# Optimization experiments

Measured on AMD Instinct MI355X. Metric: run time of the kernel, lower is better.

Reference implementation:

```python
import jax, jax.numpy as jnp
import numpy as np


def setup_inputs() -> dict:
    key = jax.random.key(0)
    k1, k2, k3 = jax.random.split(key, 3)
    B, S, D = 2, 2048, 4096
    x = jax.random.normal(k1, (B, S, D), dtype=jnp.float32)
    weight = jax.random.normal(k2, (D, D), dtype=jnp.float32)  # [out, in]
    bias = jax.random.normal(k3, (D,), dtype=jnp.float32)
    return {"x": x, "weight": weight, "bias": bias}


def reference(x, weight, bias):
    # STE binarization: forward uses sign(W) (sign(0)=0, matching torch.sign)
    w = jnp.sign(weight)
    # F.linear: x @ w.T + b
    return jnp.einsum('bsk,nk->bsn', x, w) + bias
```

## Files before the change

### kernel.cpp

```cpp
#include <hip/hip_runtime.h>
#include <hip/hip_bf16.h>
#include <stdint.h>

#define M_DIM 4096
#define N_DIM 4096
#define K_DIM 4096
#define BM 128
#define BN 128
#define BK 64

typedef float f32x4 __attribute__((ext_vector_type(4)));
typedef __bf16 bf16x8 __attribute__((ext_vector_type(8)));
typedef float f4 __attribute__((ext_vector_type(4)));
typedef unsigned int u32x4 __attribute__((ext_vector_type(4)));
typedef unsigned short u16x4 __attribute__((ext_vector_type(4)));

__device__ __forceinline__ uint16_t f32_to_bf16_rn(float f) {
  uint32_t u = __float_as_uint(f);
  u += 0x7fffu + ((u >> 16) & 1u);
  return (uint16_t)(u >> 16);
}

__global__ void convert_w_kernel(const u32x4* __restrict__ w4,
                                 u16x4* __restrict__ s4, int n4) {
  int idx = blockIdx.x * blockDim.x + threadIdx.x;
  int stride = gridDim.x * blockDim.x;
  for (int i = idx; i < n4; i += stride) {
    u32x4 v = w4[i];
    u16x4 o;
#pragma unroll
    for (int j = 0; j < 4; ++j) {
      uint32_t b = v[j];
      o[j] = ((b & 0x7fffffffu) == 0u)
                 ? (uint16_t)0
                 : (uint16_t)(0x3F80u | ((b >> 16) & 0x8000u));
    }
    s4[i] = o;
  }
}

__global__ void convert_x_kernel(const f4* __restrict__ x4,
                                 u16x4* __restrict__ hi4,
                                 u16x4* __restrict__ lo4, int n4) {
  int idx = blockIdx.x * blockDim.x + threadIdx.x;
  int stride = gridDim.x * blockDim.x;
  for (int i = idx; i < n4; i += stride) {
    f4 v = x4[i];
    u16x4 h, l;
#pragma unroll
    for (int j = 0; j < 4; ++j) {
      uint16_t hb = f32_to_bf16_rn(v[j]);
      float r = v[j] - __uint_as_float((uint32_t)hb << 16);
      h[j] = hb;
      l[j] = f32_to_bf16_rn(r);
    }
    hi4[i] = h;
    lo4[i] = l;
  }
}

__device__ __forceinline__ void gload_lds16(const void* g, void* l) {
  __builtin_amdgcn_global_load_lds(
      (__attribute__((address_space(1))) void*)(g),
      (__attribute__((address_space(3))) void*)(l),
      16, 0, 0);
}

__launch_bounds__(256, 3)
__global__ void bingemm_kernel(const uint16_t* __restrict__ Ahi,
                               const uint16_t* __restrict__ Alo,
                               const uint16_t* __restrict__ Bs,
                               const float* __restrict__ bias,
                               float* __restrict__ out) {
  __shared__ uint16_t sAh[BM * BK];
  __shared__ uint16_t sAl[BM * BK];
  __shared__ uint16_t sB[BN * BK];

  const int t = threadIdx.x;
  const int lane = t & 63;
  const int wave = t >> 6;
  const int wr = (wave >> 1) * 64;
  const int wc = (wave & 1) * 64;
  const int bm = blockIdx.y * BM;
  const int bn = blockIdx.x * BN;

  const int srow = t >> 3;
  const int scol = (t & 7) * 8;
  const uint16_t* gAh = Ahi + (size_t)(bm + srow) * K_DIM + scol;
  const uint16_t* gAl = Alo + (size_t)(bm + srow) * K_DIM + scol;
  const uint16_t* gB = Bs + (size_t)(bn + srow) * K_DIM + scol;

  f32x4 acc[4][4];
#pragma unroll
  for (int i = 0; i < 4; ++i)
#pragma unroll
    for (int j = 0; j < 4; ++j) acc[i][j] = (f32x4){0.f, 0.f, 0.f, 0.f};

  const int r15 = lane & 15;
  const int kgrp = (lane >> 4) * 8;

  for (int kt = 0; kt < K_DIM; kt += BK) {
#pragma unroll
    for (int i = 0; i < 4; ++i) {
      gload_lds16(gAh + kt + i * 32 * K_DIM, &sAh[t * 8 + i * 2048]);
      gload_lds16(gAl + kt + i * 32 * K_DIM, &sAl[t * 8 + i * 2048]);
      gload_lds16(gB + kt + i * 32 * K_DIM, &sB[t * 8 + i * 2048]);
    }
    __syncthreads();

#pragma unroll
    for (int ks = 0; ks < 2; ++ks) {
      const int ko = ks * 32 + kgrp;
      bf16x8 ah[4], al[4], bb[4];
#pragma unroll
      for (int i = 0; i < 4; ++i) {
        ah[i] = *(const bf16x8*)&sAh[(wr + i * 16 + r15) * BK + ko];
        al[i] = *(const bf16x8*)&sAl[(wr + i * 16 + r15) * BK + ko];
        bb[i] = *(const bf16x8*)&sB[(wc + i * 16 + r15) * BK + ko];
      }
#pragma unroll
      for (int mi = 0; mi < 4; ++mi)
#pragma unroll
        for (int ni = 0; ni < 4; ++ni) {
          acc[mi][ni] = __builtin_amdgcn_mfma_f32_16x16x32_bf16(
              ah[mi], bb[ni], acc[mi][ni], 0, 0, 0);
          acc[mi][ni] = __builtin_amdgcn_mfma_f32_16x16x32_bf16(
              al[mi], bb[ni], acc[mi][ni], 0, 0, 0);
        }
    }
    __syncthreads();
  }

  const int rowg = (lane >> 4) * 4;
#pragma unroll
  for (int ni = 0; ni < 4; ++ni) {
    const int col = bn + wc + ni * 16 + r15;
    const float bv = bias[col];
#pragma unroll
    for (int mi = 0; mi < 4; ++mi) {
      const int row0 = bm + wr + mi * 16 + rowg;
#pragma unroll
      for (int i = 0; i < 4; ++i)
        out[(size_t)(row0 + i) * N_DIM + col] = acc[mi][ni][i] + bv;
    }
  }
}

__global__ void fallback_gemm(const float* __restrict__ x,
                              const float* __restrict__ w,
                              const float* __restrict__ bias,
                              float* __restrict__ out) {
  __shared__ float sx[16][17];
  __shared__ float sw[16][17];
  int tx = threadIdx.x & 15, ty = threadIdx.x >> 4;
  int m = blockIdx.y * 16 + ty;
  int n = blockIdx.x * 16 + tx;
  float acc = 0.f;
  for (int k0 = 0; k0 < K_DIM; k0 += 16) {
    sx[ty][tx] = x[(size_t)m * K_DIM + k0 + tx];
    float wv = w[(size_t)(blockIdx.x * 16 + ty) * K_DIM + k0 + tx];
    sw[ty][tx] = (wv > 0.f) ? 1.f : ((wv < 0.f) ? -1.f : 0.f);
    __syncthreads();
#pragma unroll
    for (int kk = 0; kk < 16; ++kk) acc += sx[ty][kk] * sw[tx][kk];
    __syncthreads();
  }
  out[(size_t)m * N_DIM + n] = acc + bias[n];
}

extern "C" void kernel_launch(void* const* d_in, const int* in_sizes, int n_in,
                              void* d_out, int out_size, void* d_ws,
                              size_t ws_size, hipStream_t stream) {
  const float* x = (const float*)d_in[0];
  const float* w = (const float*)d_in[1];
  const float* bias = (const float*)d_in[2];
  float* out = (float*)d_out;

  const size_t elems = (size_t)N_DIM * K_DIM;
  const size_t need = elems * 2u * 3u;

  if (ws_size < need) {
    dim3 grid(N_DIM / 16, M_DIM / 16);
    fallback_gemm<<<grid, 256, 0, stream>>>(x, w, bias, out);
    return;
  }

  uint16_t* Sb = (uint16_t*)d_ws;
  uint16_t* Ahi = Sb + elems;
  uint16_t* Alo = Ahi + elems;

  const int n4 = (int)(elems / 4);
  convert_w_kernel<<<2048, 256, 0, stream>>>((const u32x4*)w, (u16x4*)Sb, n4);
  convert_x_kernel<<<2048, 256, 0, stream>>>((const f4*)x, (u16x4*)Ahi,
                                             (u16x4*)Alo, n4);

  dim3 grid(N_DIM / BN, M_DIM / BM);
  bingemm_kernel<<<grid, 256, 0, stream>>>(Ahi, Alo, Sb, bias, out);
}
```

Measured before the change: 428.0 us.

## Rewrite binary GEMM as 256x256 8-wave double-buffered kernel with concatenated hi/lo A

After: 402.8 us. 1.06x faster.

```diff
diff --git a/kernel.cpp b/kernel.cpp
--- a/kernel.cpp
+++ b/kernel.cpp
@@ -5,9 +5,7 @@
 #define M_DIM 4096
 #define N_DIM 4096
 #define K_DIM 4096
-#define BM 128
-#define BN 128
-#define BK 64
+#define NT 128
 
 typedef float f32x4 __attribute__((ext_vector_type(4)));
 typedef __bf16 bf16x8 __attribute__((ext_vector_type(8)));
@@ -40,8 +38,7 @@
 }
 
 __global__ void convert_x_kernel(const f4* __restrict__ x4,
-                                 u16x4* __restrict__ hi4,
-                                 u16x4* __restrict__ lo4, int n4) {
+                                 uint16_t* __restrict__ Ab, int n4) {
   int idx = blockIdx.x * blockDim.x + threadIdx.x;
   int stride = gridDim.x * blockDim.x;
   for (int i = idx; i < n4; i += stride) {
@@ -54,8 +51,11 @@
       h[j] = hb;
       l[j] = f32_to_bf16_rn(r);
     }
-    hi4[i] = h;
-    lo4[i] = l;
+    int flat = i * 4;
+    int m = flat >> 12;
+    int k = flat & 4095;
+    *(u16x4*)&Ab[(size_t)m * 8192 + k] = h;
+    *(u16x4*)&Ab[(size_t)m * 8192 + 4096 + k] = l;
   }
 }
 
@@ -66,82 +66,162 @@
       16, 0, 0);
 }
 
-__launch_bounds__(256, 3)
-__global__ void bingemm_kernel(const uint16_t* __restrict__ Ahi,
-                               const uint16_t* __restrict__ Alo,
-                               const uint16_t* __restrict__ Bs,
-                               const float* __restrict__ bias,
-                               float* __restrict__ out) {
-  __shared__ uint16_t sAh[BM * BK];
-  __shared__ uint16_t sAl[BM * BK];
-  __shared__ uint16_t sB[BN * BK];
+__global__ __launch_bounds__(512, 2)
+void bingemm8(const uint16_t* __restrict__ Ab, const uint16_t* __restrict__ Bs,
+              const float* __restrict__ bias, float* __restrict__ out) {
+  __shared__ uint16_t sA[2][2][8192];
+  __shared__ uint16_t sB[2][2][8192];
 
   const int t = threadIdx.x;
   const int lane = t & 63;
-  const int wave = t >> 6;
-  const int wr = (wave >> 1) * 64;
-  const int wc = (wave & 1) * 64;
-  const int bm = blockIdx.y * BM;
-  const int bn = blockIdx.x * BN;
+  const int w = t >> 6;
+  const int r15 = lane & 15;
+
+  const int bid = blockIdx.x;
+  const int swz = (bid & 7) * 32 + (bid >> 3);
+  const int bm = (swz >> 4) * 256;
+  const int bn = (swz & 15) * 256;
 
   const int srow = t >> 3;
-  const int scol = (t & 7) * 8;
-  const uint16_t* gAh = Ahi + (size_t)(bm + srow) * K_DIM + scol;
-  const uint16_t* gAl = Alo + (size_t)(bm + srow) * K_DIM + scol;
-  const uint16_t* gB = Bs + (size_t)(bn + srow) * K_DIM + scol;
-
-  f32x4 acc[4][4];
-#pragma unroll
-  for (int i = 0; i < 4; ++i)
-#pragma unroll
-    for (int j = 0; j < 4; ++j) acc[i][j] = (f32x4){0.f, 0.f, 0.f, 0.f};
-
-  const int r15 = lane & 15;
-  const int kgrp = (lane >> 4) * 8;
-
-  for (int kt = 0; kt < K_DIM; kt += BK) {
-#pragma unroll
-    for (int i = 0; i < 4; ++i) {
-      gload_lds16(gAh + kt + i * 32 * K_DIM, &sAh[t * 8 + i * 2048]);
-      gload_lds16(gAl + kt + i * 32 * K_DIM, &sAl[t * 8 + i * 2048]);
-      gload_lds16(gB + kt + i * 32 * K_DIM, &sB[t * 8 + i * 2048]);
-    }
-    __syncthreads();
-
-#pragma unroll
-    for (int ks = 0; ks < 2; ++ks) {
-      const int ko = ks * 32 + kgrp;
-      bf16x8 ah[4], al[4], bb[4];
-#pragma unroll
-      for (int i = 0; i < 4; ++i) {
-        ah[i] = *(const bf16x8*)&sAh[(wr + i * 16 + r15) * BK + ko];
-        al[i] = *(const bf16x8*)&sAl[(wr + i * 16 + r15) * BK + ko];
-        bb[i] = *(const bf16x8*)&sB[(wc + i * 16 + r15) * BK + ko];
-      }
-#pragma unroll
-      for (int mi = 0; mi < 4; ++mi)
-#pragma unroll
-        for (int ni = 0; ni < 4; ++ni) {
-          acc[mi][ni] = __builtin_amdgcn_mfma_f32_16x16x32_bf16(
-              ah[mi], bb[ni], acc[mi][ni], 0, 0, 0);
-          acc[mi][ni] = __builtin_amdgcn_mfma_f32_16x16x32_bf16(
-              al[mi], bb[ni], acc[mi][ni], 0, 0, 0);
-        }
-    }
-    __syncthreads();
-  }
+  const int scol = (((t & 7) ^ (srow & 7)) * 8);
+  const size_t aThr = (size_t)(bm + srow) * 8192 + scol;
+  const size_t bThr = (size_t)(bn + srow) * 4096 + scol;
+
+#define STAGE_A(KT, HH, BUF)                                        \
+  do {                                                              \
+    const uint16_t* g = Ab + aThr + (size_t)(HH) * 128 * 8192 +     \
+                        (size_t)(KT) * 64;                          \
+    gload_lds16(g, &sA[BUF][HH][t * 8]);                            \
+    gload_lds16(g + (size_t)64 * 8192, &sA[BUF][HH][t * 8 + 4096]); \
+  } while (0)
+#define STAGE_B(KT, HH, BUF)                                        \
+  do {                                                              \
+    const uint16_t* g = Bs + bThr + (size_t)(HH) * 128 * 4096 +     \
+                        (size_t)((KT) & 63) * 64;                   \
+    gload_lds16(g, &sB[BUF][HH][t * 8]);                            \
+    gload_lds16(g + (size_t)64 * 4096, &sB[BUF][HH][t * 8 + 4096]); \
+  } while (0)
+
+  const int klane = lane >> 4;
+  const int cb0 = (klane * 16) ^ ((lane & 7) << 4);
+  const int whA = w >> 2;
+  const int whB = (w & 3) >> 1;
+  const int wcl = (w & 1) * 64;
+  const int eA0 = r15 * 64 + (cb0 >> 1);
+  const int eA1 = eA0 ^ 32;
+  const int eB0 = (wcl + r15) * 64 + (cb0 >> 1);
+  const int eB1 = eB0 ^ 32;
+
+  bf16x8 rA[4][2], rB[4][2];
+  f32x4 acc[8][4];
+#pragma unroll
+  for (int m = 0; m < 8; ++m)
+#pragma unroll
+    for (int n = 0; n < 4; ++n) acc[m][n] = (f32x4){0.f, 0.f, 0.f, 0.f};
+
+#define LOAD_A(BUF, MOFF)                                            \
+  {                                                                  \
+    _Pragma("unroll") for (int m = 0; m < 4; ++m) {                  \
+      rA[m][0] = *(const bf16x8*)&sA[BUF][whA][eA0 + ((MOFF) + m) * 1024]; \
+      rA[m][1] = *(const bf16x8*)&sA[BUF][whA][eA1 + ((MOFF) + m) * 1024]; \
+    }                                                                \
+  }
+#define LOAD_B(BUF, NB)                                              \
+  {                                                                  \
+    _Pragma("unroll") for (int n = 0; n < 2; ++n) {                  \
+      rB[(NB) + n][0] = *(const bf16x8*)&sB[BUF][whB][eB0 + ((NB) + n) * 1024]; \
+      rB[(NB) + n][1] = *(const bf16x8*)&sB[BUF][whB][eB1 + ((NB) + n) * 1024]; \
+    }                                                                \
+  }
+#define MFMA_Q(MB, NB)                                               \
+  {                                                                  \
+    _Pragma("unroll") for (int mm = 0; mm < 4; ++mm)                 \
+    _Pragma("unroll") for (int nn = 0; nn < 2; ++nn)                 \
+    _Pragma("unroll") for (int ks = 0; ks < 2; ++ks)                 \
+      acc[(MB) + mm][(NB) + nn] = __builtin_amdgcn_mfma_f32_16x16x32_bf16( \
+          rA[mm][ks], rB[(NB) + nn][ks], acc[(MB) + mm][(NB) + nn], 0, 0, 0); \
+  }
+#define PH_PRE()                                        \
+  __builtin_amdgcn_s_barrier();                         \
+  asm volatile("s_waitcnt lgkmcnt(0)" ::: "memory");    \
+  __builtin_amdgcn_sched_barrier(0);                    \
+  __builtin_amdgcn_s_setprio(1);
+#define PH_POST()                                       \
+  __builtin_amdgcn_s_setprio(0);                        \
+  __builtin_amdgcn_s_barrier();
+#define PH_POST_VM()                                    \
+  __builtin_amdgcn_s_setprio(0);                        \
+  asm volatile("s_waitcnt vmcnt(4)" ::: "memory");      \
+  __builtin_amdgcn_s_barrier();
+
+  STAGE_B(0, 0, 0);
+  STAGE_A(0, 0, 0);
+  STAGE_B(0, 1, 0);
+  STAGE_A(0, 1, 0);
+  STAGE_B(1, 0, 1);
+  STAGE_A(1, 0, 1);
+  asm volatile("s_waitcnt vmcnt(4)" ::: "memory");
+  __builtin_amdgcn_s_barrier();
+
+  for (int i = 0; i < NT / 2; ++i) {
+    const int t1 = 2 * i + 1;
+    const int tp0 = (2 * i + 2 < NT) ? (2 * i + 2) : (NT - 1);
+    const int tp1 = (2 * i + 3 < NT) ? (2 * i + 3) : (NT - 1);
+    LOAD_A(0, 0);
+    LOAD_B(0, 0);
+    STAGE_B(t1, 1, 1);
+    PH_PRE();
+    MFMA_Q(0, 0);
+    PH_POST();
+    LOAD_B(0, 2);
+    STAGE_A(t1, 1, 1);
+    PH_PRE();
+    MFMA_Q(0, 2);
+    PH_POST();
+    LOAD_A(0, 4);
+    STAGE_B(tp0, 0, 0);
+    PH_PRE();
+    MFMA_Q(4, 2);
+    PH_POST();
+    STAGE_A(tp0, 0, 0);
+    PH_PRE();
+    MFMA_Q(4, 0);
+    PH_POST_VM();
+    LOAD_A(1, 0);
+    LOAD_B(1, 0);
+    STAGE_B(tp0, 1, 0);
+    PH_PRE();
+    MFMA_Q(0, 0);
+    PH_POST();
+    LOAD_B(1, 2);
+    STAGE_A(tp0, 1, 0);
+    PH_PRE();
+    MFMA_Q(0, 2);
+    PH_POST();
+    LOAD_A(1, 4);
+    STAGE_B(tp1, 0, 1);
+    PH_PRE();
+    MFMA_Q(4, 2);
+    PH_POST();
+    STAGE_A(tp1, 0, 1);
+    PH_PRE();
+    MFMA_Q(4, 0);
+    PH_POST_VM();
+  }
+
+  asm volatile("s_waitcnt vmcnt(0)" ::: "memory");
 
   const int rowg = (lane >> 4) * 4;
 #pragma unroll
-  for (int ni = 0; ni < 4; ++ni) {
-    const int col = bn + wc + ni * 16 + r15;
+  for (int n = 0; n < 4; ++n) {
+    const int col = bn + (w & 3) * 64 + n * 16 + r15;
     const float bv = bias[col];
 #pragma unroll
-    for (int mi = 0; mi < 4; ++mi) {
-      const int row0 = bm + wr + mi * 16 + rowg;
-#pragma unroll
-      for (int i = 0; i < 4; ++i)
-        out[(size_t)(row0 + i) * N_DIM + col] = acc[mi][ni][i] + bv;
+    for (int m = 0; m < 8; ++m) {
+      const int row0 = bm + (w >> 2) * 128 + m * 16 + rowg;
+#pragma unroll
+      for (int k = 0; k < 4; ++k)
+        out[(size_t)(row0 + k) * N_DIM + col] = acc[m][n][k] + bv;
     }
   }
 }
@@ -186,14 +266,11 @@
   }
 
   uint16_t* Sb = (uint16_t*)d_ws;
-  uint16_t* Ahi = Sb + elems;
-  uint16_t* Alo = Ahi + elems;
+  uint16_t* Ab = Sb + elems;
 
   const int n4 = (int)(elems / 4);
-  convert_w_kernel<<<2048, 256, 0, stream>>>((const u32x4*)w, (u16x4*)Sb, n4);
-  convert_x_kernel<<<2048, 256, 0, stream>>>((const f4*)x, (u16x4*)Ahi,
-                                             (u16x4*)Alo, n4);
-
-  dim3 grid(N_DIM / BN, M_DIM / BM);
-  bingemm_kernel<<<grid, 256, 0, stream>>>(Ahi, Alo, Sb, bias, out);
-}
+  convert_w_kernel<<<4096, 256, 0, stream>>>((const u32x4*)w, (u16x4*)Sb, n4);
+  convert_x_kernel<<<4096, 256, 0, stream>>>((const f4*)x, Ab, n4);
+
+  bingemm8<<<dim3(256), 512, 0, stream>>>(Ab, Sb, bias, out);
+}
```
